# Kernel optimization log

Hardware: AMD Instinct MI355X
Metric: run time of the kernel (lower is better)

## Reference

```python
import jax, jax.numpy as jnp
import numpy as np

N_EMBD = 1024
N_HEAD = 16
B, T = 4, 2048


def setup_inputs() -> dict:
    key = jax.random.key(0)
    ks = jax.random.split(key, 4)
    s = 1.0 / np.sqrt(N_EMBD)
    return {
        "x": jax.random.normal(ks[0], (B, T, N_EMBD), dtype=jnp.float32),
        "w_attn": jax.random.normal(ks[1], (N_EMBD, 3 * N_EMBD), dtype=jnp.float32) * s,
        "b_attn": jnp.zeros((3 * N_EMBD,), dtype=jnp.float32),
        "w_proj": jax.random.normal(ks[2], (N_EMBD, N_EMBD), dtype=jnp.float32) * s,
        "b_proj": jnp.zeros((N_EMBD,), dtype=jnp.float32),
    }


def reference(x, w_attn, b_attn, w_proj, b_proj):
    Bb, Tt, C = x.shape
    H = N_HEAD
    D = C // H  # head dim
    qkv = x @ w_attn + b_attn  # [B,T,3C]
    q, k, v = jnp.split(qkv, 3, axis=2)
    # [B,H,T,D]
    q = q.reshape(Bb, Tt, H, D).transpose(0, 2, 1, 3)
    k = k.reshape(Bb, Tt, H, D).transpose(0, 2, 1, 3)
    v = v.reshape(Bb, Tt, H, D).transpose(0, 2, 1, 3)
    scale = 1.0 / np.sqrt(D).astype(np.float32)
    attn = jnp.einsum("bhqd,bhkd->bhqk", q, k) * scale
    mask = jnp.tril(jnp.ones((Tt, Tt), dtype=bool))
    attn = jnp.where(mask, attn, jnp.float32(-jnp.inf))
    probs = jax.nn.softmax(attn, axis=-1)
    out = jnp.einsum("bhqk,bhkd->bhqd", probs, v)
    out = out.transpose(0, 2, 1, 3).reshape(Bb, Tt, C)
    return out @ w_proj + b_proj
```

## Files before the change

### kernel.cpp

```cpp
#include <hip/hip_runtime.h>
#include <hip/hip_bf16.h>


typedef float f32x4 __attribute__((ext_vector_type(4)));
typedef float f32x16 __attribute__((ext_vector_type(16)));
typedef short short8 __attribute__((ext_vector_type(8)));
typedef short short4v __attribute__((ext_vector_type(4)));

__device__ __forceinline__ short f2bf(float f) {
  union { __hip_bfloat16 h; short s; } u;
  u.h = __float2bfloat16(f);
  return u.s;
}

__device__ __forceinline__ void gl_lds16(const void* g, void* l) {
  __builtin_amdgcn_global_load_lds(
      (const __attribute__((address_space(1))) void*)g,
      (__attribute__((address_space(3))) void*)l, 16, 0, 0);
}

__global__ void prep(const float* __restrict__ x, const float* __restrict__ wa,
                     const float* __restrict__ wp, short* __restrict__ xb,
                     short* __restrict__ wat, short* __restrict__ wpt) {
  const int bid = blockIdx.x, tid = threadIdx.x;
  if (bid < 8192) {
    int i = (bid * 256 + tid) * 4;
    float4 v = *(const float4*)(x + i);
    short4v o;
    o[0] = f2bf(v.x); o[1] = f2bf(v.y); o[2] = f2bf(v.z); o[3] = f2bf(v.w);
    *(short4v*)(xb + i) = o;
    return;
  }
  __shared__ float tile[32][33];
  const float* in;
  short* out;
  int N, bx, by;
  if (bid < 11264) {
    int t = bid - 8192;
    in = wa; out = wat; N = 3072; bx = t % 96; by = t / 96;
  } else {
    int t = bid - 11264;
    in = wp; out = wpt; N = 1024; bx = t & 31; by = t >> 5;
  }
  int tx = tid & 31, ty = tid >> 5;
  int x0 = bx * 32, y0 = by * 32;
#pragma unroll
  for (int i = 0; i < 32; i += 8)
    tile[ty + i][tx] = in[(size_t)(y0 + ty + i) * N + x0 + tx];
  __syncthreads();
#pragma unroll
  for (int i = 0; i < 32; i += 8)
    out[(size_t)(x0 + ty + i) * 1024 + y0 + tx] = f2bf(tile[tx][ty + i]);
}


#define GEMM_BODY(A_, Bt_)                                                        \
  __shared__ __align__(16) short As[128 * 32];                                    \
  __shared__ __align__(16) short Bs[128 * 32];                                    \
  const int tid = threadIdx.x;                                                    \
  const int wv = tid >> 6;                                                        \
  const int wr = wv >> 1, wc = wv & 1;                                            \
  const int col = tid & 31, khalf = (tid >> 5) & 1;                               \
  const int m0 = blockIdx.y * 128, n0 = blockIdx.x * 128;                         \
  f32x16 acc[2][2];                                                               \
  _Pragma("unroll") for (int i = 0; i < 2; ++i)                                   \
      _Pragma("unroll") for (int j = 0; j < 2; ++j)                               \
          acc[i][j] = (f32x16)(0.f);                                              \
  for (int k0 = 0; k0 < 1024; k0 += 32) {                                         \
    _Pragma("unroll") for (int i = 0; i < 2; ++i) {                               \
      int cc = tid + i * 256;                                                     \
      int row = cc >> 2, part = ((cc & 3) - ((cc >> 3) & 3)) & 3;                 \
      gl_lds16(A_ + (size_t)(m0 + row) * 1024 + k0 + part * 8,                    \
               (char*)As + (wv * 64 + i * 256) * 16);                             \
      gl_lds16(Bt_ + (size_t)(n0 + row) * 1024 + k0 + part * 8,                   \
               (char*)Bs + (wv * 64 + i * 256) * 16);                             \
    }                                                                             \
    __syncthreads();                                                              \
    short8 af[2][2], bf[2][2];                                                    \
    _Pragma("unroll") for (int i = 0; i < 2; ++i)                                 \
        _Pragma("unroll") for (int s = 0; s < 2; ++s) {                           \
          int pa = s * 2 + khalf;                                                 \
          int ra = wr * 64 + i * 32 + col;                                        \
          int rb = wc * 64 + i * 32 + col;                                        \
          af[i][s] = *(const short8*)&As[(ra * 4 + ((pa + (ra >> 1)) & 3)) * 8];  \
          bf[i][s] = *(const short8*)&Bs[(rb * 4 + ((pa + (rb >> 1)) & 3)) * 8];  \
        }                                                                         \
    _Pragma("unroll") for (int s = 0; s < 2; ++s)                                 \
        _Pragma("unroll") for (int i = 0; i < 2; ++i)                             \
            _Pragma("unroll") for (int j = 0; j < 2; ++j)                         \
                acc[i][j] = __builtin_amdgcn_mfma_f32_32x32x16_bf16(              \
                    af[i][s], bf[j][s], acc[i][j], 0, 0, 0);                      \
    __syncthreads();                                                              \
  }

__global__ __launch_bounds__(256, 2) void gemm_qkv(
    const short* __restrict__ A, const short* __restrict__ Bt,
    const float* __restrict__ bias, short* __restrict__ Qb,
    short* __restrict__ Kb, short* __restrict__ Vtb) {
  GEMM_BODY(A, Bt)
  const int rhalf = khalf * 4;
#pragma unroll
  for (int i = 0; i < 2; ++i) {
#pragma unroll
    for (int j = 0; j < 2; ++j) {
      int n = n0 + wc * 64 + j * 32 + col;
      int n2 = n & 1023;
      int hh = n2 >> 6, d = n2 & 63;
      float bv = bias[n];
      int mb = m0 + wr * 64 + i * 32 + rhalf;
      int bb = mb >> 11;
      int bh = (bb << 4) + hh;
      if (n < 2048) {
        const bool isq = n < 1024;
#pragma unroll
        for (int a = 0; a < 16; ++a) {
          int t = (mb + (a & 3) + 8 * (a >> 2)) & 2047;
          float o = acc[i][j][a] + bv;
          size_t idx = ((size_t)bh * 2048 + t) * 64 + d;
          if (isq)
            Qb[idx] = f2bf(o * 0.18033688f);
          else
            Kb[idx] = f2bf(o);
        }
      } else {
#pragma unroll
        for (int g = 0; g < 4; ++g) {
          int t = (mb + 8 * g) & 2047;
          short4v o;
#pragma unroll
          for (int r = 0; r < 4; ++r) o[r] = f2bf(acc[i][j][g * 4 + r] + bv);
          *(short4v*)&Vtb[((size_t)bh * 64 + d) * 2048 + t] = o;
        }
      }
    }
  }
}

__global__ __launch_bounds__(256, 2) void gemm_proj(
    const short* __restrict__ A, const short* __restrict__ Bt,
    const float* __restrict__ bias, float* __restrict__ out) {
  GEMM_BODY(A, Bt)
  const int rhalf = khalf * 4;
#pragma unroll
  for (int i = 0; i < 2; ++i) {
#pragma unroll
    for (int j = 0; j < 2; ++j) {
      int n = n0 + wc * 64 + j * 32 + col;
      float bv = bias[n];
      int mb = m0 + wr * 64 + i * 32 + rhalf;
#pragma unroll
      for (int a = 0; a < 16; ++a) {
        int m = mb + (a & 3) + 8 * (a >> 2);
        out[(size_t)m * 1024 + n] = acc[i][j][a] + bv;
      }
    }
  }
}

__global__ __launch_bounds__(256, 2) void flash_attn(
    const short* __restrict__ Qg_, const short* __restrict__ Kg_,
    const short* __restrict__ Vg_, short* __restrict__ Ob) {
  constexpr int STR = 72;
  __shared__ __align__(16) short Kl[2][64 * STR];
  __shared__ __align__(16) short Vl[2][64 * STR];
  const int tid = threadIdx.x;
  const int wv = tid >> 6, ln = tid & 15, quad = (tid & 63) >> 4;
  const int bh = blockIdx.x & 63;
  const int pair = blockIdx.x >> 6;
  const short* Qg = Qg_ + (size_t)bh * 2048 * 64;
  const short* Kg = Kg_ + (size_t)bh * 2048 * 64;
  const short* Vg = Vg_ + (size_t)bh * 64 * 2048;
  const int srow = tid >> 3, spart = tid & 7;
  const int bb = bh >> 4, hh = bh & 15;

  short8 kreg[2], vreg[2];

#define LOADKV(KT)                                                              \
  {                                                                             \
    const short* Kt = Kg + (size_t)(KT) * 64 * 64;                              \
    _Pragma("unroll") for (int i = 0; i < 2; ++i) {                             \
      kreg[i] = *(const short8*)(Kt + (size_t)(srow + i * 32) * 64 + spart * 8);\
      vreg[i] = *(const short8*)(Vg + (size_t)(srow + i * 32) * 2048 +          \
                                 (KT) * 64 + spart * 8);                        \
    }                                                                           \
  }
#define WRITEKV(BUF)                                                            \
  _Pragma("unroll") for (int i = 0; i < 2; ++i) {                               \
    *(short8*)&Kl[BUF][(srow + i * 32) * STR + spart * 8] = kreg[i];            \
    *(short8*)&Vl[BUF][(srow + i * 32) * STR + spart * 8] = vreg[i];            \
  }

#pragma unroll
  for (int it = 0; it < 2; ++it) {
    const int qt = it ? pair : (15 - pair);
    const int q0 = qt * 128;
    const int qbase = q0 + wv * 32;
    const int nkt = (q0 >> 6) + 2;

    short8 qf[2][2];
#pragma unroll
    for (int h = 0; h < 2; ++h)
#pragma unroll
      for (int ch = 0; ch < 2; ++ch)
        qf[h][ch] = *(const short8*)(Qg + (size_t)(qbase + h * 16 + ln) * 64 +
                                     ch * 32 + quad * 8);

    f32x4 Oacc[2][4];
#pragma unroll
    for (int h = 0; h < 2; ++h)
#pragma unroll
      for (int mt = 0; mt < 4; ++mt) Oacc[h][mt] = (f32x4){0.f, 0.f, 0.f, 0.f};
    float lpart[2] = {0.f, 0.f};

    LOADKV(0)
    __syncthreads();
    WRITEKV(0)
    LOADKV(1)

    for (int kt = 0; kt < nkt; ++kt) {
      __syncthreads();
      const short* Kcur = Kl[kt & 1];
      const short* Vcur = Vl[kt & 1];
      if (kt + 1 < nkt) {
        WRITEKV((kt + 1) & 1)
        if (kt + 2 < nkt) LOADKV(kt + 2)
      }

      if (kt * 64 <= qbase + 31) {
        f32x4 St[2][4];
#pragma unroll
        for (int h = 0; h < 2; ++h)
#pragma unroll
          for (int kb = 0; kb < 4; ++kb) St[h][kb] = (f32x4){0.f, 0.f, 0.f, 0.f};
#pragma unroll
        for (int kb = 0; kb < 4; ++kb) {
          short8 ka0 = *(const short8*)&Kcur[(kb * 16 + ln) * STR + quad * 8];
          short8 ka1 = *(const short8*)&Kcur[(kb * 16 + ln) * STR + 32 + quad * 8];
#pragma unroll
          for (int h = 0; h < 2; ++h) {
            St[h][kb] = __builtin_amdgcn_mfma_f32_16x16x32_bf16(
                ka0, qf[h][0], St[h][kb], 0, 0, 0);
            St[h][kb] = __builtin_amdgcn_mfma_f32_16x16x32_bf16(
                ka1, qf[h][1], St[h][kb], 0, 0, 0);
          }
        }

        short4v pf[2][4];
#pragma unroll
        for (int h = 0; h < 2; ++h) {
          const bool needmask = kt * 64 + 63 > qbase + h * 16;
          const int qg = qbase + h * 16 + ln;
#pragma unroll
          for (int kb = 0; kb < 4; ++kb) {
            float p[4];
#pragma unroll
            for (int r = 0; r < 4; ++r) {
              float s = St[h][kb][r];
              if (needmask) {
                int key = kt * 64 + kb * 16 + quad * 4 + r;
                s = (key <= qg) ? s : -1e30f;
              }
              p[r] = __builtin_amdgcn_exp2f(s);
              lpart[h] += p[r];
            }
            union { __hip_bfloat162 b2; unsigned u; } w0, w1;
            w0.b2 = __float22bfloat162_rn(make_float2(p[0], p[1]));
            w1.b2 = __float22bfloat162_rn(make_float2(p[2], p[3]));
            union { short4v s4; unsigned u2[2]; } m;
            m.u2[0] = w0.u; m.u2[1] = w1.u;
            pf[h][kb] = m.s4;
          }
        }

#pragma unroll
        for (int kb = 0; kb < 4; ++kb)
#pragma unroll
          for (int mt = 0; mt < 4; ++mt) {
            short4v va =
                *(const short4v*)&Vcur[(mt * 16 + ln) * STR + kb * 16 + quad * 4];
#pragma unroll
            for (int h = 0; h < 2; ++h)
              Oacc[h][mt] = __builtin_amdgcn_mfma_f32_16x16x16bf16_1k(
                  va, pf[h][kb], Oacc[h][mt], 0, 0, 0);
          }
      }
    }

#pragma unroll
    for (int h = 0; h < 2; ++h) {
      float l = lpart[h];
      l += __shfl_xor(l, 16);
      l += __shfl_xor(l, 32);
      float rl = 1.0f / l;
      int t = qbase + h * 16 + ln;
#pragma unroll
      for (int mt = 0; mt < 4; ++mt) {
        short4v o;
#pragma unroll
        for (int r = 0; r < 4; ++r) o[r] = f2bf(Oacc[h][mt][r] * rl);
        *(short4v*)(Ob + ((size_t)(bb * 2048 + t)) * 1024 + hh * 64 + mt * 16 +
                    quad * 4) = o;
      }
    }
  }
#undef LOADKV
#undef WRITEKV
}


extern "C" void kernel_launch(void* const* d_in, const int* in_sizes, int n_in,
                              void* d_out, int out_size, void* d_ws, size_t ws_size,
                              hipStream_t stream) {
  const float* x      = (const float*)d_in[0];
  const float* w_attn = (const float*)d_in[1];
  const float* b_attn = (const float*)d_in[2];
  const float* w_proj = (const float*)d_in[3];
  const float* b_proj = (const float*)d_in[4];
  float* out = (float*)d_out;
  char* ws = (char*)d_ws;

  short* xb  = (short*)(ws);
  short* wat = (short*)(ws + 16777216);
  short* wpt = (short*)(ws + 23068672);
  short* Qb  = (short*)(ws + 25165824);
  short* Kb  = (short*)(ws + 41943040);
  short* Vtb = (short*)(ws + 58720256);
  short* Ob  = (short*)(ws + 75497472);

  prep<<<12288, 256, 0, stream>>>(x, w_attn, w_proj, xb, wat, wpt);
  gemm_qkv<<<dim3(24, 64), 256, 0, stream>>>(xb, wat, b_attn, Qb, Kb, Vtb);
  flash_attn<<<512, 256, 0, stream>>>(Qb, Kb, Vtb, Ob);
  gemm_proj<<<dim3(8, 64), 256, 0, stream>>>(Ob, wpt, b_proj, out);
}
```

Measured before the change: 263.0 us.

## Widen QKV GEMM tile to 128x256 and split softmax masking paths

The GEMM macro now takes the N tile width as a parameter. The QKV GEMM uses 128x256 tiles with four 32-wide accumulators per wave, which halves the grid and raises reuse of each A tile. In flash attention, the exp/pack loop splits into an unmasked fast path and a masked path, and the row sum uses two partial accumulators to shorten the dependency chain. The larger tile raises register and LDS use per block and gives fewer blocks, which may cost occupancy and wave balance.

```diff
diff --git a/kernel.cpp b/kernel.cpp
--- a/kernel.cpp
+++ b/kernel.cpp
@@ -54,40 +54,48 @@
 }
 
 
-#define GEMM_BODY(A_, Bt_)                                                        \
+#define GEMM_CORE(A_, Bt_, BN, JN)                                                \
   __shared__ __align__(16) short As[128 * 32];                                    \
-  __shared__ __align__(16) short Bs[128 * 32];                                    \
+  __shared__ __align__(16) short Bs[(BN) * 32];                                   \
   const int tid = threadIdx.x;                                                    \
   const int wv = tid >> 6;                                                        \
   const int wr = wv >> 1, wc = wv & 1;                                            \
   const int col = tid & 31, khalf = (tid >> 5) & 1;                               \
-  const int m0 = blockIdx.y * 128, n0 = blockIdx.x * 128;                         \
-  f32x16 acc[2][2];                                                               \
+  const int m0 = blockIdx.y * 128, n0 = blockIdx.x * (BN);                        \
+  f32x16 acc[2][JN];                                                              \
   _Pragma("unroll") for (int i = 0; i < 2; ++i)                                   \
-      _Pragma("unroll") for (int j = 0; j < 2; ++j)                               \
+      _Pragma("unroll") for (int j = 0; j < (JN); ++j)                            \
           acc[i][j] = (f32x16)(0.f);                                              \
   for (int k0 = 0; k0 < 1024; k0 += 32) {                                         \
     _Pragma("unroll") for (int i = 0; i < 2; ++i) {                               \
       int cc = tid + i * 256;                                                     \
       int row = cc >> 2, part = ((cc & 3) - ((cc >> 3) & 3)) & 3;                 \
       gl_lds16(A_ + (size_t)(m0 + row) * 1024 + k0 + part * 8,                    \
-               (char*)As + (wv * 64 + i * 256) * 16);                             \
+               (char*)As + cc * 16);                                              \
+    }                                                                             \
+    _Pragma("unroll") for (int i = 0; i < (JN); ++i) {                            \
+      int cc = tid + i * 256;                                                     \
+      int row = cc >> 2, part = ((cc & 3) - ((cc >> 3) & 3)) & 3;                 \
       gl_lds16(Bt_ + (size_t)(n0 + row) * 1024 + k0 + part * 8,                   \
-               (char*)Bs + (wv * 64 + i * 256) * 16);                             \
+               (char*)Bs + cc * 16);                                              \
     }                                                                             \
     __syncthreads();                                                              \
-    short8 af[2][2], bf[2][2];                                                    \
+    short8 af[2][2], bf[JN][2];                                                   \
     _Pragma("unroll") for (int i = 0; i < 2; ++i)                                 \
         _Pragma("unroll") for (int s = 0; s < 2; ++s) {                           \
           int pa = s * 2 + khalf;                                                 \
           int ra = wr * 64 + i * 32 + col;                                        \
-          int rb = wc * 64 + i * 32 + col;                                        \
           af[i][s] = *(const short8*)&As[(ra * 4 + ((pa + (ra >> 1)) & 3)) * 8];  \
-          bf[i][s] = *(const short8*)&Bs[(rb * 4 + ((pa + (rb >> 1)) & 3)) * 8];  \
+        }                                                                         \
+    _Pragma("unroll") for (int j = 0; j < (JN); ++j)                              \
+        _Pragma("unroll") for (int s = 0; s < 2; ++s) {                           \
+          int pa = s * 2 + khalf;                                                 \
+          int rb = wc * ((BN) / 2) + j * 32 + col;                                \
+          bf[j][s] = *(const short8*)&Bs[(rb * 4 + ((pa + (rb >> 1)) & 3)) * 8];  \
         }                                                                         \
     _Pragma("unroll") for (int s = 0; s < 2; ++s)                                 \
         _Pragma("unroll") for (int i = 0; i < 2; ++i)                             \
-            _Pragma("unroll") for (int j = 0; j < 2; ++j)                         \
+            _Pragma("unroll") for (int j = 0; j < (JN); ++j)                      \
                 acc[i][j] = __builtin_amdgcn_mfma_f32_32x32x16_bf16(              \
                     af[i][s], bf[j][s], acc[i][j], 0, 0, 0);                      \
     __syncthreads();                                                              \
@@ -97,13 +105,13 @@
     const short* __restrict__ A, const short* __restrict__ Bt,
     const float* __restrict__ bias, short* __restrict__ Qb,
     short* __restrict__ Kb, short* __restrict__ Vtb) {
-  GEMM_BODY(A, Bt)
+  GEMM_CORE(A, Bt, 256, 4)
   const int rhalf = khalf * 4;
 #pragma unroll
   for (int i = 0; i < 2; ++i) {
 #pragma unroll
-    for (int j = 0; j < 2; ++j) {
-      int n = n0 + wc * 64 + j * 32 + col;
+    for (int j = 0; j < 4; ++j) {
+      int n = n0 + wc * 128 + j * 32 + col;
       int n2 = n & 1023;
       int hh = n2 >> 6, d = n2 & 63;
       float bv = bias[n];
@@ -139,7 +147,7 @@
 __global__ __launch_bounds__(256, 2) void gemm_proj(
     const short* __restrict__ A, const short* __restrict__ Bt,
     const float* __restrict__ bias, float* __restrict__ out) {
-  GEMM_BODY(A, Bt)
+  GEMM_CORE(A, Bt, 128, 2)
   const int rhalf = khalf * 4;
 #pragma unroll
   for (int i = 0; i < 2; ++i) {
@@ -248,28 +256,45 @@
         short4v pf[2][4];
 #pragma unroll
         for (int h = 0; h < 2; ++h) {
-          const bool needmask = kt * 64 + 63 > qbase + h * 16;
-          const int qg = qbase + h * 16 + ln;
-#pragma unroll
-          for (int kb = 0; kb < 4; ++kb) {
-            float p[4];
-#pragma unroll
-            for (int r = 0; r < 4; ++r) {
-              float s = St[h][kb][r];
-              if (needmask) {
+          float lp0 = 0.f, lp1 = 0.f;
+          if (kt * 64 + 63 <= qbase + h * 16) {
+#pragma unroll
+            for (int kb = 0; kb < 4; ++kb) {
+              float p[4];
+#pragma unroll
+              for (int r = 0; r < 4; ++r)
+                p[r] = __builtin_amdgcn_exp2f(St[h][kb][r]);
+              lp0 += p[0] + p[2];
+              lp1 += p[1] + p[3];
+              union { __hip_bfloat162 b2; unsigned u; } w0, w1;
+              w0.b2 = __float22bfloat162_rn(make_float2(p[0], p[1]));
+              w1.b2 = __float22bfloat162_rn(make_float2(p[2], p[3]));
+              union { short4v s4; unsigned u2[2]; } m;
+              m.u2[0] = w0.u; m.u2[1] = w1.u;
+              pf[h][kb] = m.s4;
+            }
+          } else {
+            const int qg = qbase + h * 16 + ln;
+#pragma unroll
+            for (int kb = 0; kb < 4; ++kb) {
+              float p[4];
+#pragma unroll
+              for (int r = 0; r < 4; ++r) {
                 int key = kt * 64 + kb * 16 + quad * 4 + r;
-                s = (key <= qg) ? s : -1e30f;
+                float s = (key <= qg) ? St[h][kb][r] : -1e30f;
+                p[r] = __builtin_amdgcn_exp2f(s);
               }
-              p[r] = __builtin_amdgcn_exp2f(s);
-              lpart[h] += p[r];
+              lp0 += p[0] + p[2];
+              lp1 += p[1] + p[3];
+              union { __hip_bfloat162 b2; unsigned u; } w0, w1;
+              w0.b2 = __float22bfloat162_rn(make_float2(p[0], p[1]));
+              w1.b2 = __float22bfloat162_rn(make_float2(p[2], p[3]));
+              union { short4v s4; unsigned u2[2]; } m;
+              m.u2[0] = w0.u; m.u2[1] = w1.u;
+              pf[h][kb] = m.s4;
             }
-            union { __hip_bfloat162 b2; unsigned u; } w0, w1;
-            w0.b2 = __float22bfloat162_rn(make_float2(p[0], p[1]));
-            w1.b2 = __float22bfloat162_rn(make_float2(p[2], p[3]));
-            union { short4v s4; unsigned u2[2]; } m;
-            m.u2[0] = w0.u; m.u2[1] = w1.u;
-            pf[h][kb] = m.s4;
           }
+          lpart[h] += lp0 + lp1;
         }
 
 #pragma unroll
@@ -328,7 +353,7 @@
   short* Ob  = (short*)(ws + 75497472);
 
   prep<<<12288, 256, 0, stream>>>(x, w_attn, w_proj, xb, wat, wpt);
-  gemm_qkv<<<dim3(24, 64), 256, 0, stream>>>(xb, wat, b_attn, Qb, Kb, Vtb);
+  gemm_qkv<<<dim3(12, 64), 256, 0, stream>>>(xb, wat, b_attn, Qb, Kb, Vtb);
   flash_attn<<<512, 256, 0, stream>>>(Qb, Kb, Vtb, Ob);
   gemm_proj<<<dim3(8, 64), 256, 0, stream>>>(Ob, wpt, b_proj, out);
 }
```

New measurement: 262.3 us. No clear change (-0.3%).
